# Kernel tuning notes

Hardware: AMD Instinct MI355X
Metric: run time of the kernel (lower is better)

## Reference

```python
import jax, jax.numpy as jnp
import numpy as np

N_NODES = 100000
N_EDGES = 1600000
NUM_FEATURES = 128
DIMS = [(NUM_FEATURES, 50), (50, 50), (50, 30), (30, 30), (30, 10), (10, 10), (10, 1)]


def setup_inputs() -> dict:
    key = jax.random.key(0)
    ks = jax.random.split(key, 4 + 2 * len(DIMS))
    inp = {
        "x": jax.random.normal(ks[0], (N_NODES, NUM_FEATURES), dtype=jnp.float32),
        "edge_index": jax.random.randint(ks[1], (2, N_EDGES), 0, N_NODES, dtype=jnp.int64) if jax.config.read("jax_enable_x64") else jax.random.randint(ks[1], (2, N_EDGES), 0, N_NODES, dtype=jnp.int32),
        "edge_weight": jax.random.uniform(ks[2], (N_EDGES,), dtype=jnp.float32),
    }
    for i, (fi, fo) in enumerate(DIMS):
        scale = 1.0 / np.sqrt(fi)
        inp[f"W{i+1}"] = jax.random.normal(ks[3 + 2 * i], (fi, fo), dtype=jnp.float32) * scale
        inp[f"b{i+1}"] = jax.random.normal(ks[4 + 2 * i], (fo,), dtype=jnp.float32) * 0.01
    return inp


def _gcn_norm(edge_index, edge_weight, n):
    # Add self-loops with weight 1, then symmetric normalization (PyG GCNConv).
    loops = jnp.arange(n)
    row = jnp.concatenate([edge_index[0], loops])
    col = jnp.concatenate([edge_index[1], loops])
    w = jnp.concatenate([edge_weight, jnp.ones((n,), edge_weight.dtype)])
    deg = jnp.zeros((n,), edge_weight.dtype).at[col].add(w)
    dinv = jnp.where(deg > 0, 1.0 / jnp.sqrt(deg), 0.0)
    norm = dinv[row] * w * dinv[col]
    return row, col, norm


def _gcn_conv(x, row, col, norm, W, b):
    h = x @ W                                # [N, out]
    msg = h[row] * norm[:, None]             # gather + edge scale [E+N, out]
    out = jnp.zeros_like(h).at[col].add(msg) # scatter-add
    return out + b


def _forward(x, edge_index, edge_weight, params):
    n = x.shape[0]
    row, col, norm = _gcn_norm(edge_index, edge_weight, n)  # shared across layers
    h = x
    n_layers = len(params)
    for i, (W, b) in enumerate(params):
        h = _gcn_conv(h, row, col, norm, W, b)
        if i < n_layers - 1:
            h = jax.nn.relu(h)
        # F.dropout treated as identity (eval mode) for a deterministic reference
    return h


def reference(x, edge_index, edge_weight, W1, b1, W2, b2, W3, b3, W4, b4, W5, b5, W6, b6, W7, b7):
    params = [(W1, b1), (W2, b2), (W3, b3), (W4, b4), (W5, b5), (W6, b6), (W7, b7)]
    return _forward(x, edge_index, edge_weight, params)
```

## Files before the change

kernel.cpp:

```cpp
#include <hip/hip_runtime.h>
#include <hip/hip_fp16.h>


static constexpr int NN = 100000;
static constexpr int NE = 1600000;
static constexpr int BKL = 9;
static constexpr int NBUK = (NN + 511) >> BKL;
static constexpr int EPT = 8;
static constexpr int EB = (NE + 2047) / 2048;


__global__ __launch_bounds__(256) void k_hist0(const int* __restrict__ col,
                                               int* __restrict__ counts) {
    __shared__ int lh[NBUK];
    for (int j = threadIdx.x; j < NBUK; j += 256) lh[j] = 0;
    __syncthreads();
    int base = blockIdx.x * 2048;
#pragma unroll
    for (int k = 0; k < EPT; ++k) {
        int e = base + k * 256 + threadIdx.x;
        if (e < NE) atomicAdd(&lh[col[e] >> BKL], 1);
    }
    __syncthreads();
    for (int j = threadIdx.x; j < NBUK; j += 256)
        counts[j * EB + blockIdx.x] = lh[j];
}


__global__ __launch_bounds__(256) void k_scanA(int* __restrict__ counts,
                                               int* __restrict__ btot) {
    __shared__ int lds[256];
    const int b = blockIdx.x;
    const int t = threadIdx.x;
    int* c = counts + (size_t)b * EB;
    constexpr int PER = (EB + 255) / 256;
    int v[PER];
    int s = 0;
#pragma unroll
    for (int k = 0; k < PER; ++k) {
        int idx = t * PER + k;
        v[k] = (idx < EB) ? c[idx] : 0;
        s += v[k];
    }
    lds[t] = s;
    __syncthreads();
    for (int off = 1; off < 256; off <<= 1) {
        int u = (t >= off) ? lds[t - off] : 0;
        __syncthreads();
        lds[t] += u;
        __syncthreads();
    }
    int run = lds[t] - s;
#pragma unroll
    for (int k = 0; k < PER; ++k) {
        int idx = t * PER + k;
        if (idx < EB) { c[idx] = run; run += v[k]; }
    }
    if (t == 255) btot[b] = lds[255];
}


__global__ void k_scanB(const int* __restrict__ btot, int* __restrict__ bstart) {
    __shared__ int lds[256];
    int t = threadIdx.x;
    int v = (t < NBUK) ? btot[t] : 0;
    lds[t] = v;
    __syncthreads();
    for (int off = 1; off < 256; off <<= 1) {
        int u = (t >= off) ? lds[t - off] : 0;
        __syncthreads();
        lds[t] += u;
        __syncthreads();
    }
    if (t < NBUK) bstart[t] = lds[t] - v;
    if (t == 0) bstart[NBUK] = NE;
}


__global__ __launch_bounds__(256) void k_A1(const int* __restrict__ row,
                                            const int* __restrict__ col,
                                            const float* __restrict__ ew,
                                            const int* __restrict__ counts,
                                            const int* __restrict__ bstart,
                                            int2* __restrict__ stg) {
    __shared__ int cur[NBUK];
    for (int j = threadIdx.x; j < NBUK; j += 256)
        cur[j] = bstart[j] + counts[j * EB + blockIdx.x];
    __syncthreads();
    int base = blockIdx.x * 2048;
#pragma unroll
    for (int k = 0; k < EPT; ++k) {
        int e = base + k * 256 + threadIdx.x;
        if (e < NE) {
            int c = col[e], r = row[e];
            int pos = atomicAdd(&cur[c >> BKL], 1);
            stg[pos] = make_int2(((c & 511) << 17) | r, __float_as_int(ew[e]));
        }
    }
}


__global__ __launch_bounds__(256) void k_bdeg(const int* __restrict__ bstart,
                                              const int2* __restrict__ stg,
                                              float* __restrict__ dinv) {
    __shared__ float sdeg[512];
    const int b = blockIdx.x;
    for (int j = threadIdx.x; j < 512; j += 256) sdeg[j] = 0.0f;
    __syncthreads();
    const int s = bstart[b], e = bstart[b + 1];
    for (int p = s + threadIdx.x; p < e; p += 256) {
        int2 rec = stg[p];
        atomicAdd(&sdeg[rec.x >> 17], __int_as_float(rec.y));
    }
    __syncthreads();
    for (int j = threadIdx.x; j < 512; j += 256) {
        int idx = (b << BKL) + j;
        if (idx < NN) dinv[idx] = rsqrtf(sdeg[j] + 1.0f);
    }
}


__global__ __launch_bounds__(512) void k_place(const int* __restrict__ bstart,
                                               const int2* __restrict__ stg,
                                               const float* __restrict__ dinv,
                                               int* __restrict__ offs,
                                               int2* __restrict__ csw) {
    __shared__ int lcnt[512];
    __shared__ int cur[512];
    const int b = blockIdx.x;
    const int t = threadIdx.x;
    lcnt[t] = 0;
    __syncthreads();
    const int s = bstart[b], e = bstart[b + 1];
    for (int p = s + t; p < e; p += 512)
        atomicAdd(&lcnt[stg[p].x >> 17], 1);
    __syncthreads();
    int v = lcnt[t];
    for (int off = 1; off < 512; off <<= 1) {
        int u = (t >= off) ? lcnt[t - off] : 0;
        __syncthreads();
        lcnt[t] += u;
        __syncthreads();
    }
    int excl = lcnt[t] - v;
    int idx = (b << BKL) + t;
    if (idx <= NN) offs[idx] = s + excl;
    cur[t] = s + excl;
    __syncthreads();
    for (int p = s + t; p < e; p += 512) {
        int2 rec = stg[p];
        int cl = rec.x >> 17;
        int r = rec.x & 0x1FFFF;
        float nw = dinv[r] * __int_as_float(rec.y) * dinv[(b << BKL) + cl];
        int slot = atomicAdd(&cur[cl], 1);
        csw[slot] = make_int2(r, __float_as_int(nw));
    }
}


template <int FIN, int FOUT, int S, int NSPL>
__global__ __launch_bounds__(256, 2) void k_matmul_f(const float* __restrict__ X,
                                                     const float* __restrict__ W,
                                                     __half* __restrict__ H) {
    constexpr int FC = FOUT / NSPL;
    constexpr int NG = FIN / 16;
    const int node = blockIdx.x * 256 + threadIdx.x;
    const int ch = blockIdx.y;
    if (node >= NN) return;
    const float* xr = X + (size_t)node * FIN;
    float acc[FC];
#pragma unroll
    for (int j = 0; j < FC; ++j) acc[j] = 0.0f;

    float4 buf[2][4];
#pragma unroll
    for (int g = 0; g < 4; ++g) buf[0][g] = *(const float4*)(xr + 4 * g);
#pragma unroll
    for (int grp = 0; grp < NG; ++grp) {
        const int cur = grp & 1;
        if (grp + 1 < NG) {
#pragma unroll
            for (int g = 0; g < 4; ++g)
                buf[cur ^ 1][g] = *(const float4*)(xr + (grp + 1) * 16 + 4 * g);
        }
#pragma unroll
        for (int g = 0; g < 4; ++g)
#pragma unroll
            for (int kk = 0; kk < 4; ++kk) {
                float xv = ((const float*)&buf[cur][g])[kk];
                const float* wrow = W + (grp * 16 + 4 * g + kk) * FOUT + ch * FC;
#pragma unroll
                for (int j = 0; j < FC; ++j) acc[j] = fmaf(xv, wrow[j], acc[j]);
            }
    }
    __half* hr = H + (size_t)node * S + ch * FC;
#pragma unroll
    for (int j = 0; j < FC; ++j) hr[j] = __float2half_rn(acc[j]);
}


template <int FIN, int SX, int FOUT, int S, int NSPL>
__global__ __launch_bounds__(256, 2) void k_matmul_h(const __half* __restrict__ X,
                                                     const float* __restrict__ W,
                                                     __half* __restrict__ H) {
    constexpr int FC = FOUT / NSPL;
    constexpr int NCH = (FIN + 7) / 8;
    const int node = blockIdx.x * 256 + threadIdx.x;
    const int ch = blockIdx.y;
    if (node >= NN) return;
    const __half* xr = X + (size_t)node * SX;
    int4 raw[NCH];
#pragma unroll
    for (int c = 0; c < NCH; ++c) raw[c] = *(const int4*)(xr + 8 * c);
    float acc[FC];
#pragma unroll
    for (int j = 0; j < FC; ++j) acc[j] = 0.0f;
#pragma unroll
    for (int c = 0; c < NCH; ++c) {
        const __half2* hp = (const __half2*)&raw[c];
        const int lim = (FIN - 8 * c < 8) ? FIN - 8 * c : 8;
#pragma unroll
        for (int kk = 0; kk < 8; ++kk) {
            if (kk < lim) {
                __half2 pair = hp[kk >> 1];
                float xv = (kk & 1) ? __high2float(pair) : __low2float(pair);
                const float* wrow = W + (8 * c + kk) * FOUT + ch * FC;
#pragma unroll
                for (int j = 0; j < FC; ++j) acc[j] = fmaf(xv, wrow[j], acc[j]);
            }
        }
    }
    __half* hr = H + (size_t)node * S + ch * FC;
#pragma unroll
    for (int j = 0; j < FC; ++j) hr[j] = __float2half_rn(acc[j]);
}

__global__ void k_matmul_1h(const __half* __restrict__ X, const float* __restrict__ W,
                            float* __restrict__ H) {
    int i = blockIdx.x * blockDim.x + threadIdx.x;
    if (i >= NN) return;
    const __half* xr = X + (size_t)i * 16;
    int4 r0 = *(const int4*)xr;
    __half2 r1 = *(const __half2*)(xr + 8);
    const __half2* hp = (const __half2*)&r0;
    float acc = 0.0f;
#pragma unroll
    for (int q = 0; q < 4; ++q) {
        acc = fmaf(__low2float(hp[q]), W[2 * q], acc);
        acc = fmaf(__high2float(hp[q]), W[2 * q + 1], acc);
    }
    acc = fmaf(__low2float(r1), W[8], acc);
    acc = fmaf(__high2float(r1), W[9], acc);
    H[i] = acc;
}


static __device__ __forceinline__ int2 nt_load2(const int2* p) {
    unsigned long long raw = __builtin_nontemporal_load((const unsigned long long*)p);
    return make_int2((int)(raw & 0xFFFFFFFFull), (int)(raw >> 32));
}

template <int F, int SH, int SA, int LPN, bool RELU>
__global__ __launch_bounds__(256) void k_agg2(const int* __restrict__ offs,
                                              const int2* __restrict__ csw,
                                              const __half2* __restrict__ H,
                                              const float* __restrict__ dinv,
                                              const float* __restrict__ b,
                                              __half* __restrict__ O) {
    constexpr int R = F / 2;
    int t = blockIdx.x * blockDim.x + threadIdx.x;
    int g = t / LPN;
    int f = t - g * LPN;
    if (g >= NN) return;
    const int q0 = 4 * f;
    if (q0 >= R) return;
    int p = offs[g];
    const int pe = offs[g + 1];
    const int pl = pe - 1;

    float2 acc[4];
#pragma unroll
    for (int c = 0; c < 4; ++c) acc[c] = make_float2(0.f, 0.f);

    for (; p < pe; p += 4) {
        int2 e[4];
#pragma unroll
        for (int i = 0; i < 4; ++i) e[i] = nt_load2(csw + min(p + i, pl));
        __half2 h[4][4];
#pragma unroll
        for (int i = 0; i < 4; ++i)
            *(int4*)h[i] = *(const int4*)(H + (size_t)e[i].x * SH + q0);
#pragma unroll
        for (int i = 0; i < 4; ++i) {
            float w = (p + i < pe) ? __int_as_float(e[i].y) : 0.0f;
#pragma unroll
            for (int c = 0; c < 4; ++c) {
                acc[c].x = fmaf(__low2float(h[i][c]), w, acc[c].x);
                acc[c].y = fmaf(__high2float(h[i][c]), w, acc[c].y);
            }
        }
    }

    float di = dinv[g];
    float d2 = di * di;
    __half2 hs[4];
    *(int4*)hs = *(const int4*)(H + (size_t)g * SH + q0);
    __half2* orow = (__half2*)(O + (size_t)g * SA) + q0;
#pragma unroll
    for (int c = 0; c < 4; ++c) {
        if (q0 + c < R) {
            float vx = acc[c].x + fmaf(__low2float(hs[c]), d2, b[2 * (q0 + c)]);
            float vy = acc[c].y + fmaf(__high2float(hs[c]), d2, b[2 * (q0 + c) + 1]);
            if (RELU) { vx = fmaxf(vx, 0.f); vy = fmaxf(vy, 0.f); }
            orow[c] = __floats2half2_rn(vx, vy);
        }
    }
}

__global__ void k_agg1(const int* __restrict__ offs, const int2* __restrict__ csw,
                       const float* __restrict__ H, const float* __restrict__ dinv,
                       const float* __restrict__ b, float* __restrict__ O) {
    int g = blockIdx.x * blockDim.x + threadIdx.x;
    if (g >= NN) return;
    int p = offs[g];
    const int pe = offs[g + 1];
    const int pl = pe - 1;
    float a0 = 0.f, a1 = 0.f, a2 = 0.f, a3 = 0.f;
    for (; p < pe; p += 4) {
        int2 e0 = nt_load2(csw + min(p, pl)),     e1 = nt_load2(csw + min(p + 1, pl));
        int2 e2 = nt_load2(csw + min(p + 2, pl)), e3 = nt_load2(csw + min(p + 3, pl));
        float w0 = (p < pe)     ? __int_as_float(e0.y) : 0.f;
        float w1 = (p + 1 < pe) ? __int_as_float(e1.y) : 0.f;
        float w2 = (p + 2 < pe) ? __int_as_float(e2.y) : 0.f;
        float w3 = (p + 3 < pe) ? __int_as_float(e3.y) : 0.f;
        a0 = fmaf(H[e0.x], w0, a0);
        a1 = fmaf(H[e1.x], w1, a1);
        a2 = fmaf(H[e2.x], w2, a2);
        a3 = fmaf(H[e3.x], w3, a3);
    }
    float di = dinv[g];
    O[g] = ((a0 + a1) + (a2 + a3)) + fmaf(H[g], di * di, b[0]);
}


static inline size_t alignup(size_t x) { return (x + 255) & ~(size_t)255; }

extern "C" void kernel_launch(void* const* d_in, const int* in_sizes, int n_in,
                              void* d_out, int out_size, void* d_ws, size_t ws_size,
                              hipStream_t stream) {
    const float* x  = (const float*)d_in[0];
    const int*   ei = (const int*)d_in[1];
    const float* ew = (const float*)d_in[2];
    const float* Wp[7];
    const float* Bp[7];
    for (int l = 0; l < 7; ++l) {
        Wp[l] = (const float*)d_in[3 + 2 * l];
        Bp[l] = (const float*)d_in[4 + 2 * l];
    }
    const int* row = ei;
    const int* col = ei + NE;

    char* ws = (char*)d_ws;
    float* dinv  = (float*)ws;  ws += alignup((size_t)NN * 4);
    char*  Hb    = ws;          ws += alignup((size_t)NN * 64 * 2);
    char*  Aa    = ws;          ws += alignup((size_t)NN * 64 * 2);
    char*  Ab    = ws;          ws += alignup((size_t)NN * 64 * 2);
    int*   offs  = (int*)ws;    ws += alignup((size_t)(NN + 1) * 4);
    int*   counts= (int*)ws;    ws += alignup((size_t)NBUK * EB * 4);
    int*   btot  = (int*)ws;    ws += alignup((size_t)NBUK * 4);
    int*   bstart= (int*)ws;    ws += alignup((size_t)(NBUK + 1) * 4);
    int2*  stg   = (int2*)ws;   ws += alignup((size_t)NE * 8);
    int2*  csw   = (int2*)ws;   ws += alignup((size_t)NE * 8);

    const int gN = (NN + 255) / 256;

    k_hist0<<<EB, 256, 0, stream>>>(col, counts);
    k_scanA<<<NBUK, 256, 0, stream>>>(counts, btot);
    k_scanB<<<1, 256, 0, stream>>>(btot, bstart);
    k_A1<<<EB, 256, 0, stream>>>(row, col, ew, counts, bstart, stg);
    k_bdeg<<<NBUK, 256, 0, stream>>>(bstart, stg, dinv);
    k_place<<<NBUK, 512, 0, stream>>>(bstart, stg, dinv, offs, csw);

#define AGG(FOUT, S, LPN, RELU, OUT, LIDX)                                                  \
    k_agg2<FOUT, (S) / 2, S, LPN, RELU>                                                     \
        <<<((size_t)NN * (LPN) + 255) / 256, 256, 0, stream>>>(                             \
            offs, csw, (const __half2*)Hb, dinv, Bp[LIDX], (__half*)(OUT))

    k_matmul_f<128, 50, 64, 2><<<dim3(gN, 2), 256, 0, stream>>>(x, Wp[0], (__half*)Hb);
    AGG(50, 64, 8, true, Aa, 0);
    k_matmul_h<50, 64, 50, 64, 2><<<dim3(gN, 2), 256, 0, stream>>>((const __half*)Aa, Wp[1], (__half*)Hb);
    AGG(50, 64, 8, true, Ab, 1);
    k_matmul_h<50, 64, 30, 32, 2><<<dim3(gN, 2), 256, 0, stream>>>((const __half*)Ab, Wp[2], (__half*)Hb);
    AGG(30, 32, 4, true, Aa, 2);
    k_matmul_h<30, 32, 30, 32, 2><<<dim3(gN, 2), 256, 0, stream>>>((const __half*)Aa, Wp[3], (__half*)Hb);
    AGG(30, 32, 4, true, Ab, 3);
    k_matmul_h<30, 32, 10, 16, 1><<<dim3(gN, 1), 256, 0, stream>>>((const __half*)Ab, Wp[4], (__half*)Hb);
    AGG(10, 16, 2, true, Aa, 4);
    k_matmul_h<10, 16, 10, 16, 1><<<dim3(gN, 1), 256, 0, stream>>>((const __half*)Aa, Wp[5], (__half*)Hb);
    AGG(10, 16, 2, true, Ab, 5);
#undef AGG

    k_matmul_1h<<<gN, 256, 0, stream>>>((const __half*)Ab, Wp[6], (float*)Hb);
    k_agg1<<<gN, 256, 0, stream>>>(offs, csw, (const float*)Hb, dinv, Bp[6],
                                   (float*)d_out);
}
```

Measured before the change: 477.9 us.

## Compute full output rows per thread in dense matmuls with 64-thread blocks

The dense per-node transform kernels drop the output-column split, so each thread computes every output feature and reads its input row once rather than once per split. Blocks shrink to 64 threads, the first layer streams x with nontemporal loads in a two-buffer loop, and outputs are packed into half2 and written with vector int4 stores. The trade is larger per-thread accumulator arrays, which raise register pressure and may lower occupancy.

Result: slower. 546.9 us (+14.4%).

```diff
diff --git a/kernel.cpp b/kernel.cpp
--- a/kernel.cpp
+++ b/kernel.cpp
@@ -8,6 +8,12 @@
 static constexpr int NBUK = (NN + 511) >> BKL;
 static constexpr int EPT = 8;
 static constexpr int EB = (NE + 2047) / 2048;
+
+typedef float f4v __attribute__((ext_vector_type(4)));
+
+static __device__ __forceinline__ f4v ntld4(const float* p) {
+    return __builtin_nontemporal_load((const f4v*)p);
+}
 
 
 __global__ __launch_bounds__(256) void k_hist0(const int* __restrict__ col,
@@ -158,54 +164,65 @@
 }
 
 
-template <int FIN, int FOUT, int S, int NSPL>
-__global__ __launch_bounds__(256, 2) void k_matmul_f(const float* __restrict__ X,
-                                                     const float* __restrict__ W,
-                                                     __half* __restrict__ H) {
-    constexpr int FC = FOUT / NSPL;
+#define FMA_GROUP(BUF, KBASE)                                          \
+    _Pragma("unroll")                                                  \
+    for (int g = 0; g < 4; ++g) {                                      \
+        _Pragma("unroll")                                              \
+        for (int kk = 0; kk < 4; ++kk) {                               \
+            float xv = BUF[g][kk];                                     \
+            const float* wrow = W + ((KBASE) + 4 * g + kk) * FOUT;     \
+            _Pragma("unroll")                                          \
+            for (int j = 0; j < FOUT; ++j)                             \
+                acc[j] = fmaf(xv, wrow[j], acc[j]);                    \
+        }                                                              \
+    }
+
+template <int FIN, int FOUT, int S>
+__global__ __launch_bounds__(64) void k_matmul_f(const float* __restrict__ X,
+                                                 const float* __restrict__ W,
+                                                 __half* __restrict__ H) {
     constexpr int NG = FIN / 16;
-    const int node = blockIdx.x * 256 + threadIdx.x;
-    const int ch = blockIdx.y;
+    const int node = blockIdx.x * 64 + threadIdx.x;
     if (node >= NN) return;
     const float* xr = X + (size_t)node * FIN;
-    float acc[FC];
-#pragma unroll
-    for (int j = 0; j < FC; ++j) acc[j] = 0.0f;
-
-    float4 buf[2][4];
-#pragma unroll
-    for (int g = 0; g < 4; ++g) buf[0][g] = *(const float4*)(xr + 4 * g);
-#pragma unroll
-    for (int grp = 0; grp < NG; ++grp) {
-        const int cur = grp & 1;
-        if (grp + 1 < NG) {
-#pragma unroll
-            for (int g = 0; g < 4; ++g)
-                buf[cur ^ 1][g] = *(const float4*)(xr + (grp + 1) * 16 + 4 * g);
+    float acc[FOUT];
+#pragma unroll
+    for (int j = 0; j < FOUT; ++j) acc[j] = 0.0f;
+
+    f4v bufA[4], bufB[4];
+#pragma unroll
+    for (int g = 0; g < 4; ++g) bufA[g] = ntld4(xr + 4 * g);
+#pragma unroll 1
+    for (int grp = 0; grp < NG; grp += 2) {
+#pragma unroll
+        for (int g = 0; g < 4; ++g) bufB[g] = ntld4(xr + (grp + 1) * 16 + 4 * g);
+        FMA_GROUP(bufA, grp * 16)
+        if (grp + 2 < NG) {
+#pragma unroll
+            for (int g = 0; g < 4; ++g) bufA[g] = ntld4(xr + (grp + 2) * 16 + 4 * g);
         }
-#pragma unroll
-        for (int g = 0; g < 4; ++g)
-#pragma unroll
-            for (int kk = 0; kk < 4; ++kk) {
-                float xv = ((const float*)&buf[cur][g])[kk];
-                const float* wrow = W + (grp * 16 + 4 * g + kk) * FOUT + ch * FC;
-#pragma unroll
-                for (int j = 0; j < FC; ++j) acc[j] = fmaf(xv, wrow[j], acc[j]);
-            }
-    }
-    __half* hr = H + (size_t)node * S + ch * FC;
-#pragma unroll
-    for (int j = 0; j < FC; ++j) hr[j] = __float2half_rn(acc[j]);
-}
+        FMA_GROUP(bufB, (grp + 1) * 16)
+    }
+
+    __half2 hv[FOUT / 2];
+#pragma unroll
+    for (int j = 0; j < FOUT / 2; ++j) hv[j] = __floats2half2_rn(acc[2 * j], acc[2 * j + 1]);
+    __half* hr = H + (size_t)node * S;
+#pragma unroll
+    for (int c = 0; c < FOUT / 8; ++c) *(int4*)(hr + 8 * c) = ((const int4*)hv)[c];
+#pragma unroll
+    for (int j = (FOUT / 8) * 4; j < FOUT / 2; ++j) *(__half2*)(hr + 2 * j) = hv[j];
+}
+#undef FMA_GROUP
 
 
 template <int FIN, int SX, int FOUT, int S, int NSPL>
-__global__ __launch_bounds__(256, 2) void k_matmul_h(const __half* __restrict__ X,
-                                                     const float* __restrict__ W,
-                                                     __half* __restrict__ H) {
+__global__ __launch_bounds__(64) void k_matmul_h(const __half* __restrict__ X,
+                                                 const float* __restrict__ W,
+                                                 __half* __restrict__ H) {
     constexpr int FC = FOUT / NSPL;
     constexpr int NCH = (FIN + 7) / 8;
-    const int node = blockIdx.x * 256 + threadIdx.x;
+    const int node = blockIdx.x * 64 + threadIdx.x;
     const int ch = blockIdx.y;
     if (node >= NN) return;
     const __half* xr = X + (size_t)node * SX;
@@ -230,9 +247,14 @@
             }
         }
     }
+    __half2 hv[FC / 2];
+#pragma unroll
+    for (int j = 0; j < FC / 2; ++j) hv[j] = __floats2half2_rn(acc[2 * j], acc[2 * j + 1]);
     __half* hr = H + (size_t)node * S + ch * FC;
 #pragma unroll
-    for (int j = 0; j < FC; ++j) hr[j] = __float2half_rn(acc[j]);
+    for (int c = 0; c < FC / 8; ++c) *(int4*)(hr + 8 * c) = ((const int4*)hv)[c];
+#pragma unroll
+    for (int j = (FC / 8) * 4; j < FC / 2; ++j) *(__half2*)(hr + 2 * j) = hv[j];
 }
 
 __global__ void k_matmul_1h(const __half* __restrict__ X, const float* __restrict__ W,
@@ -372,7 +394,8 @@
     int2*  stg   = (int2*)ws;   ws += alignup((size_t)NE * 8);
     int2*  csw   = (int2*)ws;   ws += alignup((size_t)NE * 8);
 
-    const int gN = (NN + 255) / 256;
+    const int gN  = (NN + 255) / 256;
+    const int g64 = (NN + 63) / 64;
 
     k_hist0<<<EB, 256, 0, stream>>>(col, counts);
     k_scanA<<<NBUK, 256, 0, stream>>>(counts, btot);
@@ -386,17 +409,17 @@
         <<<((size_t)NN * (LPN) + 255) / 256, 256, 0, stream>>>(                             \
             offs, csw, (const __half2*)Hb, dinv, Bp[LIDX], (__half*)(OUT))
 
-    k_matmul_f<128, 50, 64, 2><<<dim3(gN, 2), 256, 0, stream>>>(x, Wp[0], (__half*)Hb);
+    k_matmul_f<128, 50, 64><<<g64, 64, 0, stream>>>(x, Wp[0], (__half*)Hb);
     AGG(50, 64, 8, true, Aa, 0);
-    k_matmul_h<50, 64, 50, 64, 2><<<dim3(gN, 2), 256, 0, stream>>>((const __half*)Aa, Wp[1], (__half*)Hb);
+    k_matmul_h<50, 64, 50, 64, 1><<<g64, 64, 0, stream>>>((const __half*)Aa, Wp[1], (__half*)Hb);
     AGG(50, 64, 8, true, Ab, 1);
-    k_matmul_h<50, 64, 30, 32, 2><<<dim3(gN, 2), 256, 0, stream>>>((const __half*)Ab, Wp[2], (__half*)Hb);
+    k_matmul_h<50, 64, 30, 32, 1><<<g64, 64, 0, stream>>>((const __half*)Ab, Wp[2], (__half*)Hb);
     AGG(30, 32, 4, true, Aa, 2);
-    k_matmul_h<30, 32, 30, 32, 2><<<dim3(gN, 2), 256, 0, stream>>>((const __half*)Aa, Wp[3], (__half*)Hb);
+    k_matmul_h<30, 32, 30, 32, 1><<<g64, 64, 0, stream>>>((const __half*)Aa, Wp[3], (__half*)Hb);
     AGG(30, 32, 4, true, Ab, 3);
-    k_matmul_h<30, 32, 10, 16, 1><<<dim3(gN, 1), 256, 0, stream>>>((const __half*)Ab, Wp[4], (__half*)Hb);
+    k_matmul_h<30, 32, 10, 16, 1><<<g64, 64, 0, stream>>>((const __half*)Ab, Wp[4], (__half*)Hb);
     AGG(10, 16, 2, true, Aa, 4);
-    k_matmul_h<10, 16, 10, 16, 1><<<dim3(gN, 1), 256, 0, stream>>>((const __half*)Aa, Wp[5], (__half*)Hb);
+    k_matmul_h<10, 16, 10, 16, 1><<<g64, 64, 0, stream>>>((const __half*)Aa, Wp[5], (__half*)Hb);
     AGG(10, 16, 2, true, Ab, 5);
 #undef AGG
 
```

## Stage first-layer input rows in LDS and split K across two waves

Applied to the files above, without the earlier changes.

The first-layer matmul (128->50) now loads 64 node rows into shared memory with coalesced float4 loads, rather than each thread streaming its own row. Each of two wavefronts computes all 50 outputs over half of K, and the partial sums are combined through LDS before packed half stores. This drops the output-channel split, so X is read once instead of twice, and global reads are coalesced. In exchange it uses 50 accumulators per thread, which adds register pressure, plus extra LDS traffic and barriers.

After: 574.5 us. 1.2x slower.

```diff
diff --git a/kernel.cpp b/kernel.cpp
--- a/kernel.cpp
+++ b/kernel.cpp
@@ -8,6 +8,8 @@
 static constexpr int NBUK = (NN + 511) >> BKL;
 static constexpr int EPT = 8;
 static constexpr int EB = (NE + 2047) / 2048;
+
+typedef float f4v __attribute__((ext_vector_type(4)));
 
 
 __global__ __launch_bounds__(256) void k_hist0(const int* __restrict__ col,
@@ -158,44 +160,91 @@
 }
 
 
-template <int FIN, int FOUT, int S, int NSPL>
-__global__ __launch_bounds__(256, 2) void k_matmul_f(const float* __restrict__ X,
+template <int FIN, int FOUT, int S>
+__global__ __launch_bounds__(128, 2) void k_matmul_f(const float* __restrict__ X,
                                                      const float* __restrict__ W,
                                                      __half* __restrict__ H) {
-    constexpr int FC = FOUT / NSPL;
-    constexpr int NG = FIN / 16;
-    const int node = blockIdx.x * 256 + threadIdx.x;
-    const int ch = blockIdx.y;
-    if (node >= NN) return;
-    const float* xr = X + (size_t)node * FIN;
-    float acc[FC];
-#pragma unroll
-    for (int j = 0; j < FC; ++j) acc[j] = 0.0f;
-
-    float4 buf[2][4];
-#pragma unroll
-    for (int g = 0; g < 4; ++g) buf[0][g] = *(const float4*)(xr + 4 * g);
-#pragma unroll
-    for (int grp = 0; grp < NG; ++grp) {
-        const int cur = grp & 1;
-        if (grp + 1 < NG) {
-#pragma unroll
-            for (int g = 0; g < 4; ++g)
-                buf[cur ^ 1][g] = *(const float4*)(xr + (grp + 1) * 16 + 4 * g);
-        }
-#pragma unroll
-        for (int g = 0; g < 4; ++g)
-#pragma unroll
-            for (int kk = 0; kk < 4; ++kk) {
-                float xv = ((const float*)&buf[cur][g])[kk];
-                const float* wrow = W + (grp * 16 + 4 * g + kk) * FOUT + ch * FC;
-#pragma unroll
-                for (int j = 0; j < FC; ++j) acc[j] = fmaf(xv, wrow[j], acc[j]);
-            }
-    }
-    __half* hr = H + (size_t)node * S + ch * FC;
-#pragma unroll
-    for (int j = 0; j < FC; ++j) hr[j] = __float2half_rn(acc[j]);
+    constexpr int ROWB = FIN * 4 + 16;
+    __shared__ __align__(16) char lds[64 * ROWB];
+    const int t = threadIdx.x;
+    const int w = t >> 6;
+    const int lane = t & 63;
+    const int nb = blockIdx.x * 64;
+
+    const float* gsrc = X + (size_t)nb * FIN;
+#pragma unroll
+    for (int m = 0; m < 16; ++m) {
+        const int n = 4 * m + (t >> 5);
+        const int g = t & 31;
+        f4v v = {0.f, 0.f, 0.f, 0.f};
+        if (nb + n < NN) v = *(const f4v*)(gsrc + n * FIN + g * 4);
+        *(f4v*)(lds + n * ROWB + g * 16) = v;
+    }
+    __syncthreads();
+
+    const char* xrow = lds + lane * ROWB + w * 256;
+    float acc[FOUT];
+#pragma unroll
+    for (int j = 0; j < FOUT; ++j) acc[j] = 0.0f;
+
+    f4v c0 = *(const f4v*)(xrow);
+    f4v c1 = *(const f4v*)(xrow + 16);
+#pragma unroll 1
+    for (int it = 0; it < 16; it += 2) {
+        f4v nx0 = c0, nx1 = c1;
+        if (it + 2 < 16) {
+            nx0 = *(const f4v*)(xrow + (it + 2) * 16);
+            nx1 = *(const f4v*)(xrow + (it + 3) * 16);
+        }
+        const float* wb = W + (64 * w + it * 4) * FOUT;
+#pragma unroll
+        for (int e = 0; e < 4; ++e)
+#pragma unroll
+            for (int j = 0; j < FOUT; ++j)
+                acc[j] = fmaf(c0[e], wb[e * FOUT + j], acc[j]);
+#pragma unroll
+        for (int e = 0; e < 4; ++e)
+#pragma unroll
+            for (int j = 0; j < FOUT; ++j)
+                acc[j] = fmaf(c1[e], wb[(4 + e) * FOUT + j], acc[j]);
+        c0 = nx0; c1 = nx1;
+    }
+
+    __syncthreads();
+    if (w == 1) {
+        float* r = (float*)(lds + lane * 208);
+#pragma unroll
+        for (int jj = 0; jj < FOUT / 4; ++jj) {
+            f4v v = {acc[4 * jj], acc[4 * jj + 1], acc[4 * jj + 2], acc[4 * jj + 3]};
+            *(f4v*)(r + 4 * jj) = v;
+        }
+#pragma unroll
+        for (int j = (FOUT / 4) * 4; j < FOUT; ++j) r[j] = acc[j];
+    }
+    __syncthreads();
+    if (w == 0) {
+        const float* r = (const float*)(lds + lane * 208);
+#pragma unroll
+        for (int jj = 0; jj < FOUT / 4; ++jj) {
+            f4v v = *(const f4v*)(r + 4 * jj);
+#pragma unroll
+            for (int e = 0; e < 4; ++e) acc[4 * jj + e] += v[e];
+        }
+#pragma unroll
+        for (int j = (FOUT / 4) * 4; j < FOUT; ++j) acc[j] += r[j];
+
+        if (nb + lane < NN) {
+            __half2 hv[FOUT / 2];
+#pragma unroll
+            for (int j = 0; j < FOUT / 2; ++j)
+                hv[j] = __floats2half2_rn(acc[2 * j], acc[2 * j + 1]);
+            __half* hr = H + (size_t)(nb + lane) * S;
+#pragma unroll
+            for (int c = 0; c < FOUT / 8; ++c) *(int4*)(hr + 8 * c) = ((const int4*)hv)[c];
+#pragma unroll
+            for (int j = (FOUT / 8) * 4; j < FOUT / 2; ++j) *(__half2*)(hr + 2 * j) = hv[j];
+        }
+    }
 }
 
 
@@ -372,7 +421,8 @@
     int2*  stg   = (int2*)ws;   ws += alignup((size_t)NE * 8);
     int2*  csw   = (int2*)ws;   ws += alignup((size_t)NE * 8);
 
-    const int gN = (NN + 255) / 256;
+    const int gN  = (NN + 255) / 256;
+    const int gB  = (NN + 63) / 64;
 
     k_hist0<<<EB, 256, 0, stream>>>(col, counts);
     k_scanA<<<NBUK, 256, 0, stream>>>(counts, btot);
@@ -386,7 +436,7 @@
         <<<((size_t)NN * (LPN) + 255) / 256, 256, 0, stream>>>(                             \
             offs, csw, (const __half2*)Hb, dinv, Bp[LIDX], (__half*)(OUT))
 
-    k_matmul_f<128, 50, 64, 2><<<dim3(gN, 2), 256, 0, stream>>>(x, Wp[0], (__half*)Hb);
+    k_matmul_f<128, 50, 64><<<gB, 128, 0, stream>>>(x, Wp[0], (__half*)Hb);
     AGG(50, 64, 8, true, Aa, 0);
     k_matmul_h<50, 64, 50, 64, 2><<<dim3(gN, 2), 256, 0, stream>>>((const __half*)Aa, Wp[1], (__half*)Hb);
     AGG(50, 64, 8, true, Ab, 1);
```
